# Kernel optimization log

Measured on AMD Instinct MI355X. Metric: run time of the kernel, lower is better.

## Reference

```python
import jax, jax.numpy as jnp
import numpy as np

EPS = 1e-12


def setup_inputs() -> dict:
    key = jax.random.key(0)
    k1, k2, k3 = jax.random.split(key, 3)
    n, in_dim, out_dim, R = 4096, 128, 128, 8
    X = jax.random.normal(k1, (n, in_dim), dtype=jnp.float32)
    A = jax.random.uniform(k2, (R, n, n), dtype=jnp.float32)
    # glorot-style scale for weights [R, out_dim, in_dim]
    scale = jnp.sqrt(6.0 / (in_dim + out_dim)).astype(jnp.float32)
    W = jax.random.uniform(k3, (R, out_dim, in_dim), minval=-1.0, maxval=1.0, dtype=jnp.float32) * scale
    return {"X": X, "A": A, "W": W}


def reference(X, A, W):
    # H[r] = X @ W[r].T  -> [R, n, out]
    H = jnp.einsum("nd,rod->rno", X, W)
    # message aggregation per relation: A[r] @ H[r] -> [R, n, out]
    M = jnp.einsum("rmn,rno->rmo", A, H)
    # row-sum degree normalization per relation (detached in original; same value in fwd)
    norms = jnp.sum(A, axis=-1, keepdims=True) + EPS  # [R, n, 1]
    out = jnp.sum(M / norms, axis=0)  # [n, out]
    return out  # activation is Identity
```

## Files before the change

### kernel.cpp

```cpp
#include <hip/hip_runtime.h>


#define N_NODES 4096
#define DIM     128
#define NREL    8
#define EPS_F   1e-12f

typedef __attribute__((ext_vector_type(4))) float f32x4;
typedef __attribute__((ext_vector_type(8))) short bf16x8;
typedef __attribute__((ext_vector_type(4))) short s16x4;
typedef __attribute__((ext_vector_type(8))) unsigned short u16x8;

__device__ __forceinline__ unsigned short f2bf(float f) {
  unsigned u = __float_as_uint(f);
  unsigned r = (u + 0x7fffu + ((u >> 16) & 1u)) >> 16;
  return (unsigned short)r;
}

__device__ __forceinline__ bf16x8 cvt8(const float* p) {
  f32x4 lo = *reinterpret_cast<const f32x4*>(p);
  f32x4 hi = *reinterpret_cast<const f32x4*>(p + 4);
  bf16x8 o;
#pragma unroll
  for (int j = 0; j < 4; ++j) { o[j] = (short)f2bf(lo[j]); o[j + 4] = (short)f2bf(hi[j]); }
  return o;
}

__global__ __launch_bounds__(256) void h_kernel(const float* __restrict__ X,
                                                const float* __restrict__ W,
                                                short* __restrict__ Ht) {
  const int r  = blockIdx.x >> 5;
  const int n0 = (blockIdx.x & 31) * 128;
  const int lane = threadIdx.x & 63;
  const int wid  = threadIdx.x >> 6;
  const int wm = wid >> 1, wn = wid & 1;
  const int l15 = lane & 15, l4 = lane >> 4;

  const float* Wr = W + (size_t)r * DIM * DIM;
  f32x4 acc[4][4] = {};

#pragma unroll
  for (int ks = 0; ks < 4; ++ks) {
    const int k = ks * 32 + l4 * 8;
    bf16x8 a[4], b[4];
#pragma unroll
    for (int mi = 0; mi < 4; ++mi)
      a[mi] = cvt8(Wr + (size_t)(wm * 64 + mi * 16 + l15) * DIM + k);
#pragma unroll
    for (int ni = 0; ni < 4; ++ni)
      b[ni] = cvt8(X + (size_t)(n0 + wn * 64 + ni * 16 + l15) * DIM + k);
#pragma unroll
    for (int mi = 0; mi < 4; ++mi)
#pragma unroll
      for (int ni = 0; ni < 4; ++ni)
        acc[mi][ni] = __builtin_amdgcn_mfma_f32_16x16x32_bf16(a[mi], b[ni], acc[mi][ni], 0, 0, 0);
  }

#pragma unroll
  for (int mi = 0; mi < 4; ++mi)
#pragma unroll
    for (int ni = 0; ni < 4; ++ni)
#pragma unroll
      for (int i = 0; i < 4; ++i) {
        const int o = wm * 64 + mi * 16 + l4 * 4 + i;
        const int n = n0 + wn * 64 + ni * 16 + l15;
        Ht[((size_t)r * DIM + o) * N_NODES + n] = (short)f2bf(acc[mi][ni][i]);
      }
}

#define BM 64
#define BK 64
#define NKT (N_NODES / BK)

__global__ __launch_bounds__(256, 2) void rgcn_main(const float* __restrict__ A,
                                                    const short* __restrict__ Ht,
                                                    float* __restrict__ out) {
  const int nwg = gridDim.x;
  const int logical = (blockIdx.x & 7) * (nwg >> 3) + (blockIdx.x >> 3);
  const int r  = logical >> 6;
  const int m0 = (logical & 63) * BM;

  const int tid  = threadIdx.x;
  const int lane = tid & 63;
  const int wid  = tid >> 6;
  const int wm = wid >> 1, wn = wid & 1;
  const int l15 = lane & 15, l4 = lane >> 4;

  const int ach = tid & 15;
  const int arb = tid >> 4;
  const int hch = tid & 7;
  const int hrb = tid >> 3;

  __shared__ short As[2][BM][72];
  __shared__ short Hs[2][DIM][72];
  __shared__ float norm_s[BM];

  const float* Ag = A + ((size_t)r * N_NODES + m0) * N_NODES;
  const short* Hg = Ht + (size_t)r * DIM * N_NODES;

  f32x4 aval[4];
  u16x8 hval[4];
  float rowsum[4] = {0.f, 0.f, 0.f, 0.f};
  f32x4 acc[2][4] = {};

  auto load_tile = [&](int kt) {
    const int k0 = kt * BK;
#pragma unroll
    for (int p = 0; p < 4; ++p)
      aval[p] = *reinterpret_cast<const f32x4*>(Ag + (size_t)(arb + 16 * p) * N_NODES + k0 + ach * 4);
#pragma unroll
    for (int q = 0; q < 4; ++q)
      hval[q] = *reinterpret_cast<const u16x8*>(Hg + (size_t)(hrb + 32 * q) * N_NODES + k0 + hch * 8);
  };

  auto store_tile = [&](int buf) {
#pragma unroll
    for (int p = 0; p < 4; ++p) {
      s16x4 b;
#pragma unroll
      for (int j = 0; j < 4; ++j) {
        b[j] = (short)f2bf(aval[p][j]);
        rowsum[p] += aval[p][j];
      }
      *reinterpret_cast<s16x4*>(&As[buf][arb + 16 * p][ach * 4]) = b;
    }
#pragma unroll
    for (int q = 0; q < 4; ++q)
      *reinterpret_cast<u16x8*>(&Hs[buf][hrb + 32 * q][hch * 8]) = hval[q];
  };

  auto compute = [&](int buf) {
#pragma unroll
    for (int ks = 0; ks < 2; ++ks) {
      bf16x8 a[2], h[4];
#pragma unroll
      for (int mi = 0; mi < 2; ++mi)
        a[mi] = *reinterpret_cast<const bf16x8*>(&As[buf][wm * 32 + mi * 16 + l15][ks * 32 + l4 * 8]);
#pragma unroll
      for (int ni = 0; ni < 4; ++ni)
        h[ni] = *reinterpret_cast<const bf16x8*>(&Hs[buf][wn * 64 + ni * 16 + l15][ks * 32 + l4 * 8]);
#pragma unroll
      for (int mi = 0; mi < 2; ++mi)
#pragma unroll
        for (int ni = 0; ni < 4; ++ni)
          acc[mi][ni] = __builtin_amdgcn_mfma_f32_16x16x32_bf16(a[mi], h[ni], acc[mi][ni], 0, 0, 0);
    }
  };

  load_tile(0);
  store_tile(0);
  __syncthreads();

  int cur = 0;
  for (int kt = 0; kt < NKT; ++kt) {
    if (kt + 1 < NKT) load_tile(kt + 1);
    compute(cur);
    if (kt + 1 < NKT) { store_tile(cur ^ 1); cur ^= 1; }
    __syncthreads();
  }

#pragma unroll
  for (int p = 0; p < 4; ++p) {
    float s = rowsum[p];
    s += __shfl_xor(s, 1);
    s += __shfl_xor(s, 2);
    s += __shfl_xor(s, 4);
    s += __shfl_xor(s, 8);
    if ((lane & 15) == 0) norm_s[arb + 16 * p] = s + EPS_F;
  }
  __syncthreads();

#pragma unroll
  for (int mi = 0; mi < 2; ++mi)
#pragma unroll
    for (int ni = 0; ni < 4; ++ni)
#pragma unroll
      for (int i = 0; i < 4; ++i) {
        const int row = wm * 32 + mi * 16 + l4 * 4 + i;
        const int col = wn * 64 + ni * 16 + l15;
        const float v = acc[mi][ni][i] / norm_s[row];
        atomicAdd(&out[(size_t)(m0 + row) * DIM + col], v);
      }
}

extern "C" void kernel_launch(void* const* d_in, const int* in_sizes, int n_in,
                              void* d_out, int out_size, void* d_ws, size_t ws_size,
                              hipStream_t stream) {
  const float* X = (const float*)d_in[0];
  const float* A = (const float*)d_in[1];
  const float* W = (const float*)d_in[2];
  float* out = (float*)d_out;
  short* Ht = (short*)d_ws;

  hipMemsetAsync(d_out, 0, (size_t)out_size * sizeof(float), stream);
  hipLaunchKernelGGL(h_kernel, dim3(NREL * (N_NODES / 128)), dim3(256), 0, stream, X, W, Ht);
  hipLaunchKernelGGL(rgcn_main, dim3(NREL * (N_NODES / BM)), dim3(256), 0, stream, A, Ht, out);
}
```

Measured before the change: 158.9 us.

## Drop LDS staging in RGCN main loop; load A and H fragments directly into registers

Each wave now owns 16 rows of A and all 128 output columns, loading A fp32 and H bf16 fragments straight from global memory into MFMA operand registers, with a manual two-stage register double buffer. This removes the shared-memory tiles, LDS writes and reads, and the per-iteration __syncthreads. The cost is that H is no longer shared across waves through LDS, so each of the four waves fetches the full H tile from global/L2 itself, and register pressure rises. The row-sum reduction now uses cross-lane shuffles and a reciprocal multiply in place of an LDS array and a division.

```diff
diff --git a/kernel.cpp b/kernel.cpp
--- a/kernel.cpp
+++ b/kernel.cpp
@@ -5,11 +5,12 @@
 #define DIM     128
 #define NREL    8
 #define EPS_F   1e-12f
+#define BM      64
+#define BK      64
+#define NKT     (N_NODES / BK)
 
 typedef __attribute__((ext_vector_type(4))) float f32x4;
 typedef __attribute__((ext_vector_type(8))) short bf16x8;
-typedef __attribute__((ext_vector_type(4))) short s16x4;
-typedef __attribute__((ext_vector_type(8))) unsigned short u16x8;
 
 __device__ __forceinline__ unsigned short f2bf(float f) {
   unsigned u = __float_as_uint(f);
@@ -68,10 +69,6 @@
       }
 }
 
-#define BM 64
-#define BK 64
-#define NKT (N_NODES / BK)
-
 __global__ __launch_bounds__(256, 2) void rgcn_main(const float* __restrict__ A,
                                                     const short* __restrict__ Ht,
                                                     float* __restrict__ out) {
@@ -80,107 +77,72 @@
   const int r  = logical >> 6;
   const int m0 = (logical & 63) * BM;
 
-  const int tid  = threadIdx.x;
-  const int lane = tid & 63;
-  const int wid  = tid >> 6;
-  const int wm = wid >> 1, wn = wid & 1;
-  const int l15 = lane & 15, l4 = lane >> 4;
+  const int lane = threadIdx.x & 63;
+  const int w    = threadIdx.x >> 6;
+  const int l15  = lane & 15, l4 = lane >> 4;
 
-  const int ach = tid & 15;
-  const int arb = tid >> 4;
-  const int hch = tid & 7;
-  const int hrb = tid >> 3;
+  const float* Arow = A + ((size_t)r * N_NODES + m0 + w * 16 + l15) * N_NODES + l4 * 8;
+  const short* Hlane = Ht + (size_t)r * DIM * N_NODES + (size_t)l15 * N_NODES + l4 * 8;
 
-  __shared__ short As[2][BM][72];
-  __shared__ short Hs[2][DIM][72];
-  __shared__ float norm_s[BM];
+  f32x4 acc[8] = {};
+  f32x4 a0[2][2], a1[2][2];
+  bf16x8 h[2][8];
+  float rs = 0.f;
 
-  const float* Ag = A + ((size_t)r * N_NODES + m0) * N_NODES;
-  const short* Hg = Ht + (size_t)r * DIM * N_NODES;
-
-  f32x4 aval[4];
-  u16x8 hval[4];
-  float rowsum[4] = {0.f, 0.f, 0.f, 0.f};
-  f32x4 acc[2][4] = {};
-
-  auto load_tile = [&](int kt) {
-    const int k0 = kt * BK;
+  auto loadA = [&](f32x4 (&dst)[2][2], int kt) {
+    const float* p = Arow + kt * BK;
 #pragma unroll
-    for (int p = 0; p < 4; ++p)
-      aval[p] = *reinterpret_cast<const f32x4*>(Ag + (size_t)(arb + 16 * p) * N_NODES + k0 + ach * 4);
+    for (int ks = 0; ks < 2; ++ks) {
+      dst[ks][0] = *reinterpret_cast<const f32x4*>(p + ks * 32);
+      dst[ks][1] = *reinterpret_cast<const f32x4*>(p + ks * 32 + 4);
+    }
+  };
+  auto loadH = [&](int kt) {
 #pragma unroll
-    for (int q = 0; q < 4; ++q)
-      hval[q] = *reinterpret_cast<const u16x8*>(Hg + (size_t)(hrb + 32 * q) * N_NODES + k0 + hch * 8);
+    for (int ks = 0; ks < 2; ++ks)
+#pragma unroll
+      for (int ni = 0; ni < 8; ++ni)
+        h[ks][ni] = *reinterpret_cast<const bf16x8*>(Hlane + (size_t)ni * 16 * N_NODES + kt * BK + ks * 32);
   };
-
-  auto store_tile = [&](int buf) {
+  auto compute = [&](f32x4 (&as)[2][2]) {
 #pragma unroll
-    for (int p = 0; p < 4; ++p) {
-      s16x4 b;
+    for (int ks = 0; ks < 2; ++ks) {
+      bf16x8 ab;
 #pragma unroll
       for (int j = 0; j < 4; ++j) {
-        b[j] = (short)f2bf(aval[p][j]);
-        rowsum[p] += aval[p][j];
+        ab[j]     = (short)f2bf(as[ks][0][j]);
+        ab[j + 4] = (short)f2bf(as[ks][1][j]);
+        rs += as[ks][0][j] + as[ks][1][j];
       }
-      *reinterpret_cast<s16x4*>(&As[buf][arb + 16 * p][ach * 4]) = b;
-    }
 #pragma unroll
-    for (int q = 0; q < 4; ++q)
-      *reinterpret_cast<u16x8*>(&Hs[buf][hrb + 32 * q][hch * 8]) = hval[q];
-  };
-
-  auto compute = [&](int buf) {
-#pragma unroll
-    for (int ks = 0; ks < 2; ++ks) {
-      bf16x8 a[2], h[4];
-#pragma unroll
-      for (int mi = 0; mi < 2; ++mi)
-        a[mi] = *reinterpret_cast<const bf16x8*>(&As[buf][wm * 32 + mi * 16 + l15][ks * 32 + l4 * 8]);
-#pragma unroll
-      for (int ni = 0; ni < 4; ++ni)
-        h[ni] = *reinterpret_cast<const bf16x8*>(&Hs[buf][wn * 64 + ni * 16 + l15][ks * 32 + l4 * 8]);
-#pragma unroll
-      for (int mi = 0; mi < 2; ++mi)
-#pragma unroll
-        for (int ni = 0; ni < 4; ++ni)
-          acc[mi][ni] = __builtin_amdgcn_mfma_f32_16x16x32_bf16(a[mi], h[ni], acc[mi][ni], 0, 0, 0);
+      for (int ni = 0; ni < 8; ++ni)
+        acc[ni] = __builtin_amdgcn_mfma_f32_16x16x32_bf16(ab, h[ks][ni], acc[ni], 0, 0, 0);
     }
   };
 
-  load_tile(0);
-  store_tile(0);
-  __syncthreads();
-
-  int cur = 0;
-  for (int kt = 0; kt < NKT; ++kt) {
-    if (kt + 1 < NKT) load_tile(kt + 1);
-    compute(cur);
-    if (kt + 1 < NKT) { store_tile(cur ^ 1); cur ^= 1; }
-    __syncthreads();
+  loadA(a0, 0);
+  for (int kt = 0; kt < NKT; kt += 2) {
+    loadH(kt);
+    loadA(a1, kt + 1);
+    compute(a0);
+    loadH(kt + 1);
+    if (kt + 2 < NKT) loadA(a0, kt + 2);
+    compute(a1);
   }
 
+  rs += __shfl_xor(rs, 16);
+  rs += __shfl_xor(rs, 32);
+  float ninv[4];
 #pragma unroll
-  for (int p = 0; p < 4; ++p) {
-    float s = rowsum[p];
-    s += __shfl_xor(s, 1);
-    s += __shfl_xor(s, 2);
-    s += __shfl_xor(s, 4);
-    s += __shfl_xor(s, 8);
-    if ((lane & 15) == 0) norm_s[arb + 16 * p] = s + EPS_F;
-  }
-  __syncthreads();
+  for (int i = 0; i < 4; ++i)
+    ninv[i] = 1.0f / (__shfl(rs, l4 * 4 + i) + EPS_F);
 
+  float* orow = out + (size_t)(m0 + w * 16) * DIM;
 #pragma unroll
-  for (int mi = 0; mi < 2; ++mi)
+  for (int ni = 0; ni < 8; ++ni)
 #pragma unroll
-    for (int ni = 0; ni < 4; ++ni)
-#pragma unroll
-      for (int i = 0; i < 4; ++i) {
-        const int row = wm * 32 + mi * 16 + l4 * 4 + i;
-        const int col = wn * 64 + ni * 16 + l15;
-        const float v = acc[mi][ni][i] / norm_s[row];
-        atomicAdd(&out[(size_t)(m0 + row) * DIM + col], v);
-      }
+    for (int i = 0; i < 4; ++i)
+      atomicAdd(&orow[(size_t)(l4 * 4 + i) * DIM + ni * 16 + l15], acc[ni][i] * ninv[i]);
 }
 
 extern "C" void kernel_launch(void* const* d_in, const int* in_sizes, int n_in,
```

New measurement: 324.8 us. 104% more time.
